# Optimization experiments

Hardware: AMD Instinct MI355X
Metric: run time of the kernel (lower is better)

The kernel has to match this reference:

```python
import jax, jax.numpy as jnp
import numpy as np

S, N, MSA_DIM, PAIR_DIM, D, H = 8, 256, 256, 128, 32, 8
EPS = 1e-5


def layer_norm(x, w, b):
    mu = jnp.mean(x, axis=-1, keepdims=True)
    var = jnp.mean((x - mu) ** 2, axis=-1, keepdims=True)
    return (x - mu) * jax.lax.rsqrt(var + EPS) * w + b


def setup_inputs() -> dict:
    key = jax.random.key(0)
    ks = jax.random.split(key, 8)
    def rnd(k, shape, scale=1.0):
        return jax.random.normal(k, shape, jnp.float32) * scale
    return {
        "msa_rep": rnd(ks[0], (S, N, MSA_DIM)),
        "pair_rep": rnd(ks[1], (N, N, PAIR_DIM)),
        "ln_w": jnp.ones((MSA_DIM,), jnp.float32),
        "ln_b": jnp.zeros((MSA_DIM,), jnp.float32),
        "w_qkv": rnd(ks[2], (MSA_DIM, 3 * H * D), 0.02),
        "ln_pair_w": jnp.ones((PAIR_DIM,), jnp.float32),
        "ln_pair_b": jnp.zeros((PAIR_DIM,), jnp.float32),
        "w_b": rnd(ks[3], (PAIR_DIM, H), 0.02),
        "w_g": rnd(ks[4], (MSA_DIM, H * D), 0.02),
        "w_out": rnd(ks[5], (H * D, MSA_DIM), 0.02),
        "b_out": jnp.zeros((MSA_DIM,), jnp.float32),
    }


def reference(msa_rep, pair_rep, ln_w, ln_b, w_qkv, ln_pair_w, ln_pair_b,
              w_b, w_g, w_out, b_out):
    s, n, _ = msa_rep.shape
    x = layer_norm(msa_rep, ln_w, ln_b)                      # [s, n, msa_dim]
    qkv = x @ w_qkv                                          # [s, n, 3*h*d]
    # chunk(3, dim=-1) then view(..., d, h): d outer, h inner
    q, k, v = [t.reshape(s, n, D, H) for t in jnp.split(qkv, 3, axis=-1)]
    # pair bias: LN + linear -> [n, n, h], broadcast to [1, i, j, 1, h]
    b = layer_norm(pair_rep, ln_pair_w, ln_pair_b) @ w_b     # [n, n, h]
    g = jax.nn.sigmoid(x @ w_g).reshape(s, n, D, H)          # gate [s, n, d, h]
    # NOTE: logits keep the d axis (no contraction): einsum 'sidh,sjdh->sijdh'
    scores = (q[:, :, None, :, :] * k[:, None, :, :, :]) * (D ** -0.5) \
             + b[None, :, :, None, :]                        # [s, i, j, d, h]
    a = jax.nn.softmax(scores, axis=2)                       # softmax over j
    out = g * jnp.einsum('sijdh,sjdh->sidh', a, v)           # [s, n, d, h]
    return out.reshape(s, n, D * H) @ w_out + b_out          # [s, n, msa_dim]
```

## Files before the change

### kernel.cpp

```cpp
#include <hip/hip_runtime.h>
#include <math.h>

#define S_DIM 8
#define N_RES 256
#define MSA_DIM 256
#define PAIR_DIM 128
#define D_DIM 32
#define H_DIM 8
#define M_ROWS (S_DIM * N_RES)
#define QKV_N (3 * H_DIM * D_DIM)
#define HD (H_DIM * D_DIM)
#define XW_N 1024
#define LOG2E 1.4426950408889634f

typedef __attribute__((ext_vector_type(8))) short short8;
typedef __attribute__((ext_vector_type(4))) float floatx4;

#define DPP_ADD(x, ctrl, rmask)                                                \
    x += __int_as_float(__builtin_amdgcn_update_dpp(                           \
        0, __float_as_int(x), (ctrl), (rmask), 0xf, true))

__device__ __forceinline__ float wave_sum63(float x) {
    DPP_ADD(x, 0x111, 0xf);
    DPP_ADD(x, 0x112, 0xf);
    DPP_ADD(x, 0x114, 0xf);
    DPP_ADD(x, 0x118, 0xf);
    DPP_ADD(x, 0x142, 0xa);
    DPP_ADD(x, 0x143, 0xc);
    return x;
}

__device__ __forceinline__ float quad_sum(float x) {
    x += __int_as_float(__builtin_amdgcn_update_dpp(
        0, __float_as_int(x), 0xB1, 0xf, 0xf, true));
    x += __int_as_float(__builtin_amdgcn_update_dpp(
        0, __float_as_int(x), 0x4E, 0xf, 0xf, true));
    return x;
}

__device__ __forceinline__ unsigned short bf16rn(float v) {
    unsigned u = __float_as_uint(v);
    return (unsigned short)((u + 0x7FFF + ((u >> 16) & 1)) >> 16);
}

__global__ __launch_bounds__(256) void prep_kernel(
    const float* __restrict__ w_qkv, const float* __restrict__ w_g,
    unsigned short* __restrict__ whiT, unsigned short* __restrict__ wloT,
    const float* __restrict__ w_out,
    unsigned short* __restrict__ wouthiT, unsigned short* __restrict__ woutloT,
    const float* __restrict__ msa, const float* __restrict__ lnw,
    const float* __restrict__ lnb, unsigned short* __restrict__ xhi,
    unsigned short* __restrict__ xlo)
{
    int b = blockIdx.x;
    int t = threadIdx.x;

    {
        int wv = t >> 6, l = t & 63;
        int row = b * 4 + wv;
        float4 v4 = *(const float4*)&msa[(size_t)row * 256 + l * 4];
        float s1 = v4.x + v4.y + v4.z + v4.w;
        float s2 = v4.x * v4.x + v4.y * v4.y + v4.z * v4.z + v4.w * v4.w;
        s1 = wave_sum63(s1);
        s2 = wave_sum63(s2);
        float S1 = __int_as_float(__builtin_amdgcn_readlane(__float_as_int(s1), 63));
        float S2 = __int_as_float(__builtin_amdgcn_readlane(__float_as_int(s2), 63));
        float mu = S1 * (1.0f / 256.0f);
        float var = S2 * (1.0f / 256.0f) - mu * mu;
        float rs = rsqrtf(var + 1e-5f);
        float4 w4 = *(const float4*)&lnw[l * 4];
        float4 bb4 = *(const float4*)&lnb[l * 4];
        float y[4];
        y[0] = (v4.x - mu) * rs * w4.x + bb4.x;
        y[1] = (v4.y - mu) * rs * w4.y + bb4.y;
        y[2] = (v4.z - mu) * rs * w4.z + bb4.z;
        y[3] = (v4.w - mu) * rs * w4.w + bb4.w;
        unsigned short hh[4], ll[4];
#pragma unroll
        for (int i = 0; i < 4; i++) {
            hh[i] = bf16rn(y[i]);
            ll[i] = bf16rn(y[i] - __uint_as_float((unsigned)hh[i] << 16));
        }
        uint2 ph, pl;
        ph.x = (unsigned)hh[0] | ((unsigned)hh[1] << 16);
        ph.y = (unsigned)hh[2] | ((unsigned)hh[3] << 16);
        pl.x = (unsigned)ll[0] | ((unsigned)ll[1] << 16);
        pl.y = (unsigned)ll[2] | ((unsigned)ll[3] << 16);
        *(uint2*)&xhi[(size_t)row * 256 + l * 4] = ph;
        *(uint2*)&xlo[(size_t)row * 256 + l * 4] = pl;
    }

    if (t < 64) {
        int id = b * 64 + t;
        int n = id >> 5, oct = id & 31, k0 = oct * 8;
        const float* src;
        int stride;
        if (n < QKV_N) { src = w_qkv + n; stride = QKV_N; }
        else           { src = w_g + (n - QKV_N); stride = HD; }
        unsigned short h8[8], l8[8];
#pragma unroll
        for (int j = 0; j < 8; j++) {
            float v = src[(size_t)(k0 + j) * stride];
            unsigned short h = bf16rn(v);
            h8[j] = h;
            l8[j] = bf16rn(v - __uint_as_float((unsigned)h << 16));
        }
        *(short8*)&whiT[n * 256 + k0] = *(short8*)h8;
        *(short8*)&wloT[n * 256 + k0] = *(short8*)l8;
    } else if (t < 80) {
        int id = b * 16 + (t - 64);
        int n = id >> 5, oct = id & 31, k0 = oct * 8;
        unsigned short h8[8], l8[8];
#pragma unroll
        for (int j = 0; j < 8; j++) {
            int k = k0 + j;
            int wrow = (k & 31) * 8 + (k >> 5);
            float v = w_out[(size_t)wrow * 256 + n];
            unsigned short h = bf16rn(v);
            h8[j] = h;
            l8[j] = bf16rn(v - __uint_as_float((unsigned)h << 16));
        }
        *(short8*)&wouthiT[n * 256 + k0] = *(short8*)h8;
        *(short8*)&woutloT[n * 256 + k0] = *(short8*)l8;
    }
}

__global__ __launch_bounds__(256) void mid_kernel(
    const float* __restrict__ pair, const float* __restrict__ lw,
    const float* __restrict__ lb, const float* __restrict__ wb,
    float* __restrict__ b2,
    const unsigned short* __restrict__ xhi, const unsigned short* __restrict__ xlo,
    const unsigned short* __restrict__ whiT, const unsigned short* __restrict__ wloT,
    float* __restrict__ q_t, float* __restrict__ k_t,
    float* __restrict__ v_t, float* __restrict__ g_t)
{
    __shared__ __align__(16) char smem[35840];
    int bx = blockIdx.x;
    int t = threadIdx.x;
    int g3 = bx / 3, r3 = bx - g3 * 3;

    if (r3 != 2) {
        float* As = (float*)smem;
        float* Spart = (float*)smem + 1552;
        float* Qpart = (float*)smem + 1816;
        int pair_id = g3 * 2 + r3;
        if (t < 128) {
            float lwc = lw[t];
#pragma unroll
            for (int h = 0; h < 8; h++)
                As[t * 12 + h] = lwc * wb[t * 8 + h] * LOG2E;
        }
        __syncthreads();
        {
            int h = t >> 5, seg = t & 31, cbase = seg * 4;
            float sa = 0, sq = 0;
#pragma unroll
            for (int cc = 0; cc < 4; cc++) {
                int c = cbase + cc;
                sa += As[c * 12 + h];
                sq += lb[c] * wb[c * 8 + h];
            }
            Spart[h * 33 + seg] = sa;
            Qpart[h * 33 + seg] = sq * LOG2E;
        }
        __syncthreads();
        if (t < 8) {
            float s = 0, q = 0;
#pragma unroll
            for (int j = 0; j < 32; j++) {
                s += Spart[t * 33 + j];
                q += Qpart[t * 33 + j];
            }
            As[1536 + t] = s;
            As[1544 + t] = q;
        }
        __syncthreads();
        int row = pair_id * 64 + (t >> 2);
        int q = t & 3;
        const float* in = pair + (size_t)row * PAIR_DIM;
        float4 x4[8];
#pragma unroll
        for (int it = 0; it < 8; it++)
            x4[it] = *(const float4*)&in[it * 16 + q * 4];
        float s = 0, s2 = 0;
        float dot[8] = {};
#pragma unroll
        for (int it = 0; it < 8; it++) {
            float xk[4];
            *(float4*)xk = x4[it];
#pragma unroll
            for (int k = 0; k < 4; k++) {
                int c = it * 16 + q * 4 + k;
                float xv = xk[k];
                s += xv; s2 += xv * xv;
                float4 A0 = *(const float4*)&As[c * 12];
                float4 A1 = *(const float4*)&As[c * 12 + 4];
                dot[0] += xv * A0.x; dot[1] += xv * A0.y;
                dot[2] += xv * A0.z; dot[3] += xv * A0.w;
                dot[4] += xv * A1.x; dot[5] += xv * A1.y;
                dot[6] += xv * A1.z; dot[7] += xv * A1.w;
            }
        }
        s = quad_sum(s);
        s2 = quad_sum(s2);
#pragma unroll
        for (int h = 0; h < 8; h++) dot[h] = quad_sum(dot[h]);
        float mu = s * (1.0f / 128.0f);
        float var = s2 * (1.0f / 128.0f) - mu * mu;
        float rs = rsqrtf(var + 1e-5f);
        int h0 = q * 2;
#pragma unroll
        for (int u = 0; u < 2; u++) {
            int h = h0 + u;
            b2[h * 65536 + row] = rs * (dot[h] - mu * As[1536 + h]) + As[1544 + h];
        }
    } else {
        unsigned short* As = (unsigned short*)smem;
        unsigned short* Bs = As + 64 * 72;
        float* Cs = (float*)(smem + 18432);
        int gid = g3;
        int n0 = (gid & 15) * 64, m0 = (gid >> 4) * 64;
        int w = t >> 6, L = t & 63;
        int wm = (w & 1) * 32, wn = (w >> 1) * 32;
        int l15 = L & 15, l4 = L >> 4;
        int alm = t >> 3, alk = (t & 7) * 8;
        floatx4 acc[2][2];
#pragma unroll
        for (int a = 0; a < 2; a++)
#pragma unroll
            for (int c = 0; c < 2; c++) acc[a][c] = (floatx4){0, 0, 0, 0};

        short8 pa0 = *(const short8*)&xhi[(m0 + alm) * 256 + alk];
        short8 pa1 = *(const short8*)&xhi[(m0 + alm + 32) * 256 + alk];
        short8 pb[2];
#pragma unroll
        for (int j = 0; j < 2; j++) {
            int id = t + 256 * j;
            int bn = id >> 3, bc = (id & 7) * 8;
            pb[j] = *(const short8*)&whiT[(n0 + bn) * 256 + bc];
        }

        for (int r = 0; r < 12; r++) {
            __syncthreads();
            *(short8*)&As[alm * 72 + alk] = pa0;
            *(short8*)&As[(alm + 32) * 72 + alk] = pa1;
#pragma unroll
            for (int j = 0; j < 2; j++) {
                int id = t + 256 * j;
                int bn = id >> 3, bc = (id & 7) * 8;
                *(short8*)&Bs[bn * 72 + bc] = pb[j];
            }
            __syncthreads();
            if (r < 11) {
                int rn = r + 1;
                int seg = rn >> 2, kb = (rn & 3) * 64;
                const unsigned short* An = (seg == 1) ? xlo : xhi;
                const unsigned short* Bn = (seg == 2) ? wloT : whiT;
                pa0 = *(const short8*)&An[(m0 + alm) * 256 + kb + alk];
                pa1 = *(const short8*)&An[(m0 + alm + 32) * 256 + kb + alk];
#pragma unroll
                for (int j = 0; j < 2; j++) {
                    int id = t + 256 * j;
                    int bn = id >> 3, bc = (id & 7) * 8;
                    pb[j] = *(const short8*)&Bn[(n0 + bn) * 256 + kb + bc];
                }
            }
#pragma unroll
            for (int ks = 0; ks < 2; ks++) {
                int ko = ks * 32 + l4 * 8;
                short8 af[2], bf[2];
#pragma unroll
                for (int a = 0; a < 2; a++)
                    af[a] = *(short8*)&As[(wm + a * 16 + l15) * 72 + ko];
#pragma unroll
                for (int c = 0; c < 2; c++)
                    bf[c] = *(short8*)&Bs[(wn + c * 16 + l15) * 72 + ko];
#pragma unroll
                for (int a = 0; a < 2; a++)
#pragma unroll
                    for (int c = 0; c < 2; c++)
                        acc[a][c] = __builtin_amdgcn_mfma_f32_16x16x32_bf16(
                            af[a], bf[c], acc[a][c], 0, 0, 0);
            }
        }
#pragma unroll
        for (int a = 0; a < 2; a++)
#pragma unroll
            for (int c = 0; c < 2; c++) {
                int nl = wn + c * 16 + l15;
#pragma unroll
                for (int rg = 0; rg < 4; rg++) {
                    int ml = wm + a * 16 + l4 * 4 + rg;
                    Cs[ml * 68 + nl] = acc[a][c][rg];
                }
            }
        __syncthreads();
        int qkv_mode = (n0 < QKV_N);
        int chunk = n0 >> 8;
        int dbase = (n0 & 255) >> 3;
#pragma unroll
        for (int j = 0; j < 4; j++) {
            int id = t + 256 * j;
            int m = id >> 4;
            int h = (id >> 1) & 7;
            int dq = id & 1;
            float vals[4];
#pragma unroll
            for (int jj = 0; jj < 4; jj++)
                vals[jj] = Cs[m * 68 + (dq * 4 + jj) * 8 + h];
            int mm = m0 + m;
            int daddr = dbase + dq * 4;
            if (qkv_mode) {
                float* dst = (chunk == 0) ? q_t : ((chunk == 1) ? k_t : v_t);
                *(float4*)&dst[(size_t)(h * M_ROWS + mm) * D_DIM + daddr] =
                    *(float4*)vals;
            } else {
                float4 o;
                o.x = 1.0f / (1.0f + __expf(-vals[0]));
                o.y = 1.0f / (1.0f + __expf(-vals[1]));
                o.z = 1.0f / (1.0f + __expf(-vals[2]));
                o.w = 1.0f / (1.0f + __expf(-vals[3]));
                *(float4*)&g_t[(size_t)(h * M_ROWS + mm) * D_DIM + daddr] = o;
            }
        }
    }
}

__global__ __launch_bounds__(256) void attn_kernel(
    const float* __restrict__ q_t, const float* __restrict__ k_t,
    const float* __restrict__ v_t, const float* __restrict__ g_t,
    const float* __restrict__ b2, unsigned short* __restrict__ ao_hi,
    unsigned short* __restrict__ ao_lo)
{
    __shared__ float k_sh[256][32];
    __shared__ float v_sh[256][32];
    int blk = blockIdx.x;
    int h = blk & 7, s = (blk >> 3) & 7, it = blk >> 6;
    int t = threadIdx.x;
    const float* kb = k_t + (size_t)(h * M_ROWS + s * N_RES) * D_DIM;
    const float* vb = v_t + (size_t)(h * M_ROWS + s * N_RES) * D_DIM;
    for (int idx = t; idx < 2048; idx += 256) {
        ((float4*)k_sh)[idx] = ((const float4*)kb)[idx];
        ((float4*)v_sh)[idx] = ((const float4*)vb)[idx];
    }
    __syncthreads();
    int jp = t & 3, dg = (t >> 2) & 7, li = t >> 5;
    int d0 = dg * 4;
    const float SCL2 = 0.17677669529663687f * LOG2E;
    int ig[4], mrow[4];
    float qs[4][4];
#pragma unroll
    for (int r = 0; r < 4; r++) {
        ig[r] = it * 32 + r * 8 + li;
        mrow[r] = s * N_RES + ig[r];
        float4 q4 = *(const float4*)&q_t[(size_t)(h * M_ROWS + mrow[r]) * D_DIM + d0];
        qs[r][0] = q4.x * SCL2; qs[r][1] = q4.y * SCL2;
        qs[r][2] = q4.z * SCL2; qs[r][3] = q4.w * SCL2;
    }
    float den[4][4] = {}, acc[4][4] = {};
    const float* bbase = b2 + h * 65536;
    for (int js4 = 0; js4 < 16; js4++) {
        float bb[4][4];
#pragma unroll
        for (int r = 0; r < 4; r++)
            *(float4*)&bb[r][0] =
                *(const float4*)&bbase[ig[r] * 256 + jp * 64 + js4 * 4];
#pragma unroll
        for (int u = 0; u < 4; u++) {
            int j = jp * 64 + js4 * 4 + u;
            float ka[4], va[4];
            *(float4*)ka = *(const float4*)&k_sh[j][d0];
            *(float4*)va = *(const float4*)&v_sh[j][d0];
#pragma unroll
            for (int r = 0; r < 4; r++) {
#pragma unroll
                for (int c = 0; c < 4; c++) {
                    float e = __builtin_amdgcn_exp2f(qs[r][c] * ka[c] + bb[r][u]);
                    den[r][c] += e;
                    acc[r][c] += e * va[c];
                }
            }
        }
    }
#pragma unroll
    for (int r = 0; r < 4; r++)
#pragma unroll
        for (int c = 0; c < 4; c++) {
            den[r][c] = quad_sum(den[r][c]);
            acc[r][c] = quad_sum(acc[r][c]);
        }
    if (jp == 0) {
#pragma unroll
        for (int r = 0; r < 4; r++) {
            float4 g4 = *(const float4*)&g_t[(size_t)(h * M_ROWS + mrow[r]) * D_DIM + d0];
            float o[4];
            o[0] = g4.x * acc[r][0] * __builtin_amdgcn_rcpf(den[r][0]);
            o[1] = g4.y * acc[r][1] * __builtin_amdgcn_rcpf(den[r][1]);
            o[2] = g4.z * acc[r][2] * __builtin_amdgcn_rcpf(den[r][2]);
            o[3] = g4.w * acc[r][3] * __builtin_amdgcn_rcpf(den[r][3]);
            unsigned short hi[4], lo[4];
#pragma unroll
            for (int c = 0; c < 4; c++) {
                hi[c] = bf16rn(o[c]);
                lo[c] = bf16rn(o[c] - __uint_as_float((unsigned)hi[c] << 16));
            }
            size_t base = (size_t)mrow[r] * 256 + h * 32 + d0;
            uint2 ph, pl;
            ph.x = (unsigned)hi[0] | ((unsigned)hi[1] << 16);
            ph.y = (unsigned)hi[2] | ((unsigned)hi[3] << 16);
            pl.x = (unsigned)lo[0] | ((unsigned)lo[1] << 16);
            pl.y = (unsigned)lo[2] | ((unsigned)lo[3] << 16);
            *(uint2*)&ao_hi[base] = ph;
            *(uint2*)&ao_lo[base] = pl;
        }
    }
}

__global__ __launch_bounds__(256) void out_mfma_kernel(
    const unsigned short* __restrict__ ahi, const unsigned short* __restrict__ alo,
    const unsigned short* __restrict__ whi, const unsigned short* __restrict__ wlo,
    const float* __restrict__ bias, float* __restrict__ out)
{
    __shared__ unsigned short As[32 * 72];
    __shared__ unsigned short Bs[64 * 72];
    __shared__ float Cs[32 * 68];
    int t = threadIdx.x;
    int n0 = blockIdx.x * 64, m0 = blockIdx.y * 32;
    int w = t >> 6, L = t & 63;
    int wm = (w & 1) * 16, wn = (w >> 1) * 32;
    int l15 = L & 15, l4 = L >> 4;
    int alm = t >> 3, alk = (t & 7) * 8;
    floatx4 acc[2];
#pragma unroll
    for (int b = 0; b < 2; b++) acc[b] = (floatx4){0, 0, 0, 0};

    short8 pa0 = *(const short8*)&ahi[(m0 + alm) * 256 + alk];
    short8 pb[2];
#pragma unroll
    for (int j = 0; j < 2; j++) {
        int id = t + 256 * j;
        int bn = id >> 3, bc = (id & 7) * 8;
        pb[j] = *(const short8*)&whi[(n0 + bn) * 256 + bc];
    }

    for (int r = 0; r < 12; r++) {
        __syncthreads();
        *(short8*)&As[alm * 72 + alk] = pa0;
#pragma unroll
        for (int j = 0; j < 2; j++) {
            int id = t + 256 * j;
            int bn = id >> 3, bc = (id & 7) * 8;
            *(short8*)&Bs[bn * 72 + bc] = pb[j];
        }
        __syncthreads();
        if (r < 11) {
            int rn = r + 1;
            int seg = rn >> 2, kb = (rn & 3) * 64;
            const unsigned short* An = (seg == 1) ? alo : ahi;
            const unsigned short* Bn = (seg == 2) ? wlo : whi;
            pa0 = *(const short8*)&An[(m0 + alm) * 256 + kb + alk];
#pragma unroll
            for (int j = 0; j < 2; j++) {
                int id = t + 256 * j;
                int bn = id >> 3, bc = (id & 7) * 8;
                pb[j] = *(const short8*)&Bn[(n0 + bn) * 256 + kb + bc];
            }
        }
#pragma unroll
        for (int ks = 0; ks < 2; ks++) {
            int ko = ks * 32 + l4 * 8;
            short8 af, bf[2];
            af = *(short8*)&As[(wm + l15) * 72 + ko];
#pragma unroll
            for (int b = 0; b < 2; b++)
                bf[b] = *(short8*)&Bs[(wn + b * 16 + l15) * 72 + ko];
#pragma unroll
            for (int b = 0; b < 2; b++)
                acc[b] = __builtin_amdgcn_mfma_f32_16x16x32_bf16(
                    af, bf[b], acc[b], 0, 0, 0);
        }
    }
#pragma unroll
    for (int b = 0; b < 2; b++) {
        int nl = wn + b * 16 + l15;
#pragma unroll
        for (int rg = 0; rg < 4; rg++) {
            int ml = wm + l4 * 4 + rg;
            Cs[ml * 68 + nl] = acc[b][rg];
        }
    }
    __syncthreads();
#pragma unroll
    for (int j = 0; j < 2; j++) {
        int id = t + 256 * j;
        int m = id >> 4, nc = (id & 15) * 4;
        float4 v = *(float4*)&Cs[m * 68 + nc];
        float4 bb = *(const float4*)&bias[n0 + nc];
        float4 o;
        o.x = v.x + bb.x; o.y = v.y + bb.y;
        o.z = v.z + bb.z; o.w = v.w + bb.w;
        *(float4*)&out[(size_t)(m0 + m) * 256 + n0 + nc] = o;
    }
}

extern "C" void kernel_launch(void* const* d_in, const int* in_sizes, int n_in,
                              void* d_out, int out_size, void* d_ws, size_t ws_size,
                              hipStream_t stream)
{
    const float* msa_rep   = (const float*)d_in[0];
    const float* pair_rep  = (const float*)d_in[1];
    const float* ln_w      = (const float*)d_in[2];
    const float* ln_b      = (const float*)d_in[3];
    const float* w_qkv     = (const float*)d_in[4];
    const float* ln_pair_w = (const float*)d_in[5];
    const float* ln_pair_b = (const float*)d_in[6];
    const float* w_b       = (const float*)d_in[7];
    const float* w_g       = (const float*)d_in[8];
    const float* w_out     = (const float*)d_in[9];
    const float* b_out     = (const float*)d_in[10];
    float* out = (float*)d_out;

    float* ws = (float*)d_ws;
    const size_t CH = 524288;
    float* q_t = ws + 0 * CH;
    float* k_t = ws + 1 * CH;
    float* v_t = ws + 2 * CH;
    float* g_t = ws + 3 * CH;
    float* b2  = ws + 4 * CH;
    unsigned short* ao_hi   = (unsigned short*)(ws + 5 * CH);
    unsigned short* ao_lo   = ao_hi + (size_t)M_ROWS * 256;
    unsigned short* xhi     = (unsigned short*)(ws + 6 * CH);
    unsigned short* xlo     = xhi + (size_t)M_ROWS * 256;
    unsigned short* whiT    = (unsigned short*)(ws + 7 * CH);
    unsigned short* wloT    = whiT + (size_t)XW_N * 256;
    unsigned short* wouthiT = (unsigned short*)(ws + 8 * CH);
    unsigned short* woutloT = wouthiT + 65536;

    prep_kernel<<<512, 256, 0, stream>>>(
        w_qkv, w_g, whiT, wloT,
        w_out, wouthiT, woutloT,
        msa_rep, ln_w, ln_b, xhi, xlo);

    mid_kernel<<<1536, 256, 0, stream>>>(
        pair_rep, ln_pair_w, ln_pair_b, w_b, b2,
        xhi, xlo, whiT, wloT, q_t, k_t, v_t, g_t);

    attn_kernel<<<512, 256, 0, stream>>>(q_t, k_t, v_t, g_t, b2, ao_hi, ao_lo);

    out_mfma_kernel<<<dim3(4, 64), 256, 0, stream>>>(
        ao_hi, ao_lo, wouthiT, woutloT, b_out, out);
}
```

Baseline: 149.2 us.

## Prefetch pair-bias and gate in attention, double-buffer output GEMM with smaller tiles

In the attention kernel the pair-bias loads are software-prefetched one iteration ahead, and the gate load is hoisted before the quad reductions so its latency overlaps them. The output GEMM moves to 16-row tiles with double-buffered shared memory, one sync per k-step, and twice as many blocks. This targets exposed memory latency and low occupancy in the small final GEMM. The cost is more registers in attention and more redundant B-tile loads across blocks in the GEMM.

```diff
diff --git a/kernel.cpp b/kernel.cpp
--- a/kernel.cpp
+++ b/kernel.cpp
@@ -359,12 +359,20 @@
     }
     float den[4][4] = {}, acc[4][4] = {};
     const float* bbase = b2 + h * 65536;
+    float4 bbv[4];
+#pragma unroll
+    for (int r = 0; r < 4; r++)
+        bbv[r] = *(const float4*)&bbase[ig[r] * 256 + jp * 64];
     for (int js4 = 0; js4 < 16; js4++) {
         float bb[4][4];
 #pragma unroll
         for (int r = 0; r < 4; r++)
-            *(float4*)&bb[r][0] =
-                *(const float4*)&bbase[ig[r] * 256 + jp * 64 + js4 * 4];
+            *(float4*)&bb[r][0] = bbv[r];
+        if (js4 < 15) {
+#pragma unroll
+            for (int r = 0; r < 4; r++)
+                bbv[r] = *(const float4*)&bbase[ig[r] * 256 + jp * 64 + (js4 + 1) * 4];
+        }
 #pragma unroll
         for (int u = 0; u < 4; u++) {
             int j = jp * 64 + js4 * 4 + u;
@@ -382,6 +390,10 @@
             }
         }
     }
+    float4 g4[4];
+#pragma unroll
+    for (int r = 0; r < 4; r++)
+        g4[r] = *(const float4*)&g_t[(size_t)(h * M_ROWS + mrow[r]) * D_DIM + d0];
 #pragma unroll
     for (int r = 0; r < 4; r++)
 #pragma unroll
@@ -392,12 +404,11 @@
     if (jp == 0) {
 #pragma unroll
         for (int r = 0; r < 4; r++) {
-            float4 g4 = *(const float4*)&g_t[(size_t)(h * M_ROWS + mrow[r]) * D_DIM + d0];
             float o[4];
-            o[0] = g4.x * acc[r][0] * __builtin_amdgcn_rcpf(den[r][0]);
-            o[1] = g4.y * acc[r][1] * __builtin_amdgcn_rcpf(den[r][1]);
-            o[2] = g4.z * acc[r][2] * __builtin_amdgcn_rcpf(den[r][2]);
-            o[3] = g4.w * acc[r][3] * __builtin_amdgcn_rcpf(den[r][3]);
+            o[0] = g4[r].x * acc[r][0] * __builtin_amdgcn_rcpf(den[r][0]);
+            o[1] = g4[r].y * acc[r][1] * __builtin_amdgcn_rcpf(den[r][1]);
+            o[2] = g4[r].z * acc[r][2] * __builtin_amdgcn_rcpf(den[r][2]);
+            o[3] = g4[r].w * acc[r][3] * __builtin_amdgcn_rcpf(den[r][3]);
             unsigned short hi[4], lo[4];
 #pragma unroll
             for (int c = 0; c < 4; c++) {
@@ -421,44 +432,41 @@
     const unsigned short* __restrict__ whi, const unsigned short* __restrict__ wlo,
     const float* __restrict__ bias, float* __restrict__ out)
 {
-    __shared__ unsigned short As[32 * 72];
-    __shared__ unsigned short Bs[64 * 72];
-    __shared__ float Cs[32 * 68];
+    __shared__ unsigned short As[2][16 * 72];
+    __shared__ unsigned short Bs[2][64 * 72];
+    __shared__ float Cs[16 * 68];
     int t = threadIdx.x;
-    int n0 = blockIdx.x * 64, m0 = blockIdx.y * 32;
+    int n0 = blockIdx.x * 64, m0 = blockIdx.y * 16;
     int w = t >> 6, L = t & 63;
-    int wm = (w & 1) * 16, wn = (w >> 1) * 32;
+    int wn = w * 16;
     int l15 = L & 15, l4 = L >> 4;
     int alm = t >> 3, alk = (t & 7) * 8;
-    floatx4 acc[2];
-#pragma unroll
-    for (int b = 0; b < 2; b++) acc[b] = (floatx4){0, 0, 0, 0};
-
-    short8 pa0 = *(const short8*)&ahi[(m0 + alm) * 256 + alk];
-    short8 pb[2];
+    bool doA = (t < 128);
+    floatx4 acc = (floatx4){0, 0, 0, 0};
+
+    short8 pa, pb[2];
+    if (doA) pa = *(const short8*)&ahi[(m0 + alm) * 256 + alk];
 #pragma unroll
     for (int j = 0; j < 2; j++) {
         int id = t + 256 * j;
         int bn = id >> 3, bc = (id & 7) * 8;
         pb[j] = *(const short8*)&whi[(n0 + bn) * 256 + bc];
     }
+    if (doA) *(short8*)&As[0][alm * 72 + alk] = pa;
+#pragma unroll
+    for (int j = 0; j < 2; j++) {
+        int id = t + 256 * j;
+        int bn = id >> 3, bc = (id & 7) * 8;
+        *(short8*)&Bs[0][bn * 72 + bc] = pb[j];
+    }
 
     for (int r = 0; r < 12; r++) {
-        __syncthreads();
-        *(short8*)&As[alm * 72 + alk] = pa0;
-#pragma unroll
-        for (int j = 0; j < 2; j++) {
-            int id = t + 256 * j;
-            int bn = id >> 3, bc = (id & 7) * 8;
-            *(short8*)&Bs[bn * 72 + bc] = pb[j];
-        }
-        __syncthreads();
         if (r < 11) {
             int rn = r + 1;
             int seg = rn >> 2, kb = (rn & 3) * 64;
             const unsigned short* An = (seg == 1) ? alo : ahi;
             const unsigned short* Bn = (seg == 2) ? wlo : whi;
-            pa0 = *(const short8*)&An[(m0 + alm) * 256 + kb + alk];
+            if (doA) pa = *(const short8*)&An[(m0 + alm) * 256 + kb + alk];
 #pragma unroll
             for (int j = 0; j < 2; j++) {
                 int id = t + 256 * j;
@@ -466,34 +474,32 @@
                 pb[j] = *(const short8*)&Bn[(n0 + bn) * 256 + kb + bc];
             }
         }
+        __syncthreads();
+        int cur = r & 1;
 #pragma unroll
         for (int ks = 0; ks < 2; ks++) {
             int ko = ks * 32 + l4 * 8;
-            short8 af, bf[2];
-            af = *(short8*)&As[(wm + l15) * 72 + ko];
-#pragma unroll
-            for (int b = 0; b < 2; b++)
-                bf[b] = *(short8*)&Bs[(wn + b * 16 + l15) * 72 + ko];
-#pragma unroll
-            for (int b = 0; b < 2; b++)
-                acc[b] = __builtin_amdgcn_mfma_f32_16x16x32_bf16(
-                    af, bf[b], acc[b], 0, 0, 0);
-        }
-    }
-#pragma unroll
-    for (int b = 0; b < 2; b++) {
-        int nl = wn + b * 16 + l15;
-#pragma unroll
-        for (int rg = 0; rg < 4; rg++) {
-            int ml = wm + l4 * 4 + rg;
-            Cs[ml * 68 + nl] = acc[b][rg];
-        }
-    }
+            short8 af = *(short8*)&As[cur][l15 * 72 + ko];
+            short8 bf = *(short8*)&Bs[cur][(wn + l15) * 72 + ko];
+            acc = __builtin_amdgcn_mfma_f32_16x16x32_bf16(af, bf, acc, 0, 0, 0);
+        }
+        if (r < 11) {
+            int nxt = cur ^ 1;
+            if (doA) *(short8*)&As[nxt][alm * 72 + alk] = pa;
+#pragma unroll
+            for (int j = 0; j < 2; j++) {
+                int id = t + 256 * j;
+                int bn = id >> 3, bc = (id & 7) * 8;
+                *(short8*)&Bs[nxt][bn * 72 + bc] = pb[j];
+            }
+        }
+    }
+#pragma unroll
+    for (int rg = 0; rg < 4; rg++)
+        Cs[(l4 * 4 + rg) * 68 + wn + l15] = acc[rg];
     __syncthreads();
-#pragma unroll
-    for (int j = 0; j < 2; j++) {
-        int id = t + 256 * j;
-        int m = id >> 4, nc = (id & 15) * 4;
+    {
+        int m = t >> 4, nc = (t & 15) * 4;
         float4 v = *(float4*)&Cs[m * 68 + nc];
         float4 bb = *(const float4*)&bias[n0 + nc];
         float4 o;
@@ -547,6 +553,6 @@
 
     attn_kernel<<<512, 256, 0, stream>>>(q_t, k_t, v_t, g_t, b2, ao_hi, ao_lo);
 
-    out_mfma_kernel<<<dim3(4, 64), 256, 0, stream>>>(
+    out_mfma_kernel<<<dim3(4, 128), 256, 0, stream>>>(
         ao_hi, ao_lo, wouthiT, woutloT, b_out, out);
 }
```

After: 143.9 us. -3.6%, faster.
